# Optimization experiments

Hardware: AMD Instinct MI355X
Metric: run time of the kernel (lower is better)

Reference implementation:

```python
import jax, jax.numpy as jnp
import numpy as np

N = 100000
E = 1600000
NFEAT = 256
NHID = 128


def setup_inputs() -> dict:
    key = jax.random.key(0)
    k1, k2, k3, k4 = jax.random.split(key, 4)
    x = jax.random.normal(k1, (N, NFEAT), dtype=jnp.float32)
    edge_index = jax.random.randint(k2, (2, E), 0, N, dtype=jnp.int64)
    # GCNConv linear weight (stored as [nfeat, nhid] so h = x @ W) + bias
    W = jax.random.normal(k3, (NFEAT, NHID), dtype=jnp.float32) / np.sqrt(NFEAT)
    b = jnp.zeros((NHID,), dtype=jnp.float32)
    # PReLU single shared slope parameter (torch default init 0.25)
    prelu_a = jnp.asarray(0.25, dtype=jnp.float32)
    return {"x": x, "edge_index": edge_index, "W": W, "b": b, "prelu_a": prelu_a}


def _gcn_prelu(x, edge_index, W, b, prelu_a):
    n = x.shape[0]
    # spectral_norm reparametrization: divide weight by its largest singular value
    sigma = jnp.linalg.norm(W.astype(jnp.float32), ord=2)
    h = x @ (W / sigma)  # [N, nhid]
    # add self-loops (PyG GCNConv default)
    loop = jnp.arange(n, dtype=edge_index.dtype)
    row = jnp.concatenate([edge_index[0], loop])  # source
    col = jnp.concatenate([edge_index[1], loop])  # destination
    # symmetric degree normalization: deg from destination counts
    deg = jax.ops.segment_sum(jnp.ones_like(col, dtype=h.dtype), col, num_segments=n)
    dinv = jnp.where(deg > 0, jax.lax.rsqrt(deg), 0.0)
    norm = dinv[row] * dinv[col]  # [E+N]
    msgs = h[row] * norm[:, None]  # [E+N, nhid] gather
    out = jax.ops.segment_sum(msgs, col, num_segments=n) + b  # scatter-add
    # PReLU with shared slope
    return jnp.where(out > 0, out, prelu_a * out)


def reference(x, edge_index, W, b, prelu_a):
    return _gcn_prelu(x, edge_index, W, b, prelu_a)
```

## Files before the change

kernel.cpp:

```cpp
#include <hip/hip_runtime.h>

#define NN 100000
#define EE 1600000
#define NF 256
#define NH 128

#define BK 98
#define BNODE 1024
#define CHUNK 4096
#define NCHUNK ((EE + CHUNK - 1) / CHUNK)
#define CAP 24576

typedef unsigned int u32;
typedef unsigned short u16;
typedef __attribute__((ext_vector_type(8))) short short8;
typedef __attribute__((ext_vector_type(4))) float f32x4;

static __device__ __forceinline__ u16 f2bf(float f) {
  u32 u = __float_as_uint(f);
  u32 r = (u + 0x7FFFu + ((u >> 16) & 1u)) >> 16;
  return (u16)r;
}
static __device__ __forceinline__ float bflo(u32 u) { return __uint_as_float(u << 16); }
static __device__ __forceinline__ float bfhi(u32 u) { return __uint_as_float(u & 0xFFFF0000u); }

__global__ __launch_bounds__(256) void k_p0(const int* __restrict__ col,
                                            u32* __restrict__ hist2d) {
  __shared__ u32 hist[BK];
  int t = threadIdx.x;
  if (t < BK) hist[t] = 0;
  __syncthreads();
  int e0 = blockIdx.x * CHUNK;
  int e1 = min(e0 + CHUNK, EE);
  for (int e = e0 + t; e < e1; e += 256) {
    u32 d = (u32)col[e];
    atomicAdd(&hist[d >> 10], 1u);
  }
  __syncthreads();
  if (t < BK) hist2d[blockIdx.x * BK + t] = hist[t];
}

__global__ __launch_bounds__(256) void k_bs_spec(const u32* __restrict__ hist2d,
                                                 u32* __restrict__ bcnt,
                                                 u32* __restrict__ bbase,
                                                 u32* __restrict__ gcur,
                                                 u32* __restrict__ off,
                                                 const float* __restrict__ W,
                                                 u16* __restrict__ WtG,
                                                 float* __restrict__ sig) {
  __shared__ __align__(16) char MB[65536];
  __shared__ float diag[128];
  __shared__ float red[256];
  __shared__ float uvec[128];
  __shared__ float itrS;
  __shared__ int jmS;
  int t = threadIdx.x;

  if (blockIdx.x == 0) {
    u32* c = (u32*)MB;
    if (t < BK) {
      u32 s = 0;
      for (int ch = 0; ch < NCHUNK; ch++) s += hist2d[ch * BK + t];
      c[t] = s;
    }
    __syncthreads();
    if (t == 0) {
      u32 s = 0;
      for (int b2 = 0; b2 < BK; b2++) {
        bcnt[b2] = c[b2];
        bbase[b2] = s;
        gcur[b2] = s;
        s += c[b2];
      }
      off[NN] = EE;
    }
    return;
  }

  int l = t & 63, w = t >> 6;
  int p = l & 15, q = l >> 4;

  for (int base = t * 4; base < NF * NH; base += 256 * 4) {
    float4 v = *(const float4*)&W[base];
    int k = base >> 7, c0 = base & 127;
#pragma unroll
    for (int i = 0; i < 4; i++) {
      int c = c0 + i;
      int inner = (k * 2) ^ ((c & 7) << 4);
      *(u16*)(MB + c * 512 + inner) = f2bf(((const float*)&v)[i]);
    }
  }
  __syncthreads();
  for (int g = t; g < 128 * 128; g += 256) {
    int c = g >> 7, k = (g & 127) * 2;
    u32 val = *(u32*)(MB + c * 512 + ((k * 2) ^ ((c & 7) << 4)));
    ((u32*)WtG)[g] = val;
  }

  f32x4 acc[2][8] = {};
#pragma unroll
  for (int ks = 0; ks < 8; ks++) {
    int kb = (ks * 32 + q * 8) * 2;
    short8 afr[2], bfr[8];
#pragma unroll
    for (int m = 0; m < 2; m++) {
      int ra = w * 32 + m * 16 + p;
      afr[m] = *(const short8*)(MB + ra * 512 + (kb ^ ((ra & 7) << 4)));
    }
#pragma unroll
    for (int n = 0; n < 8; n++) {
      int r = n * 16 + p;
      bfr[n] = *(const short8*)(MB + r * 512 + (kb ^ ((r & 7) << 4)));
    }
#pragma unroll
    for (int m = 0; m < 2; m++)
#pragma unroll
      for (int n = 0; n < 8; n++)
        acc[m][n] = __builtin_amdgcn_mfma_f32_16x16x32_bf16(afr[m], bfr[n], acc[m][n], 0, 0, 0);
  }
#pragma unroll
  for (int m = 0; m < 2; m++)
#pragma unroll
    for (int n = 0; n < 8; n++)
#pragma unroll
      for (int g = 0; g < 4; g++) {
        int r = w * 32 + m * 16 + q * 4 + g;
        int c = n * 16 + p;
        if (r == c) diag[r] = acc[m][n][g];
      }
  __syncthreads();
  if (t == 0) {
    float s = 0.f;
    for (int i = 0; i < 128; i++) s += diag[i];
    itrS = 1.0f / s;
  }
  __syncthreads();
  {
    float itr = itrS;
    char* mb0 = MB;
#pragma unroll
    for (int m = 0; m < 2; m++)
#pragma unroll
      for (int n = 0; n < 8; n++)
#pragma unroll
        for (int g = 0; g < 4; g++) {
          int r = w * 32 + m * 16 + q * 4 + g;
          int c = n * 16 + p;
          *(u16*)(mb0 + r * 256 + ((c * 2) ^ ((r & 7) << 4))) = f2bf(acc[m][n][g] * itr);
        }
  }

  char* src = MB;
  char* dst = MB + 32768;
  for (int s = 0; s < 8; s++) {
    __syncthreads();
    f32x4 mac[2][8] = {};
#pragma unroll
    for (int ks = 0; ks < 4; ks++) {
      int kb = (ks * 32 + q * 8) * 2;
      short8 afr[2], bfr[8];
#pragma unroll
      for (int m = 0; m < 2; m++) {
        int ra = w * 32 + m * 16 + p;
        afr[m] = *(const short8*)(src + ra * 256 + (kb ^ ((ra & 7) << 4)));
      }
#pragma unroll
      for (int n = 0; n < 8; n++) {
        int r = n * 16 + p;
        bfr[n] = *(const short8*)(src + r * 256 + (kb ^ ((r & 7) << 4)));
      }
#pragma unroll
      for (int m = 0; m < 2; m++)
#pragma unroll
        for (int n = 0; n < 8; n++)
          mac[m][n] = __builtin_amdgcn_mfma_f32_16x16x32_bf16(afr[m], bfr[n], mac[m][n], 0, 0, 0);
    }
#pragma unroll
    for (int m = 0; m < 2; m++)
#pragma unroll
      for (int n = 0; n < 8; n++)
#pragma unroll
        for (int g = 0; g < 4; g++) {
          int r = w * 32 + m * 16 + q * 4 + g;
          int c = n * 16 + p;
          if (r == c) diag[r] = mac[m][n][g];
        }
    __syncthreads();
    if (t == 0) {
      float ss = 0.f;
      for (int i = 0; i < 128; i++) ss += diag[i];
      itrS = 1.0f / ss;
    }
    __syncthreads();
    float it2 = itrS;
#pragma unroll
    for (int m = 0; m < 2; m++)
#pragma unroll
      for (int n = 0; n < 8; n++)
#pragma unroll
        for (int g = 0; g < 4; g++) {
          int r = w * 32 + m * 16 + q * 4 + g;
          int c = n * 16 + p;
          *(u16*)(dst + r * 256 + ((c * 2) ^ ((r & 7) << 4))) = f2bf(mac[m][n][g] * it2);
        }
    char* tmp = src; src = dst; dst = tmp;
  }
  __syncthreads();

  if (t == 0) {
    int jm = 0;
    float bm = diag[0];
    for (int i = 1; i < 128; i++)
      if (diag[i] > bm) { bm = diag[i]; jm = i; }
    jmS = jm;
  }
  __syncthreads();
  int jm = jmS;
  if (t < 128) {
    u16 hv = *(u16*)(src + jm * 256 + ((t * 2) ^ ((jm & 7) << 4)));
    uvec[t] = __uint_as_float(((u32)hv) << 16);
  }
  __syncthreads();
  {
    float a2 = 0.f;
    const float* wr = &W[t * NH];
    for (int k = 0; k < NH; k++) a2 += wr[k] * uvec[k];
    red[t] = a2 * a2;
  }
  __syncthreads();
  if (t == 0) {
    float num = 0.f;
    for (int i = 0; i < 256; i++) num += red[i];
    float den = 0.f;
    for (int i = 0; i < 128; i++) den += uvec[i] * uvec[i];
    sig[0] = rsqrtf(num / den);
  }
}

__global__ __launch_bounds__(256) void k_p1(const int* __restrict__ row,
                                            const int* __restrict__ col,
                                            u32* __restrict__ gcur,
                                            u32* __restrict__ binned) {
  __shared__ u32 keybuf[CHUNK];
  __shared__ unsigned char bktbuf[CHUNK];
  __shared__ u32 hist[BK], lstart[BK], lofs[BK], gb[BK];
  int t = threadIdx.x;
  if (t < BK) hist[t] = 0;
  __syncthreads();
  int e0 = blockIdx.x * CHUNK;
  int n = min(CHUNK, EE - e0);
  for (int i = t; i < n; i += 256) {
    u32 d = (u32)col[e0 + i];
    atomicAdd(&hist[d >> 10], 1u);
  }
  __syncthreads();
  if (t == 0) {
    u32 s = 0;
    for (int b = 0; b < BK; b++) { lstart[b] = s; lofs[b] = s; s += hist[b]; }
  }
  __syncthreads();
  if (t < BK && hist[t]) gb[t] = atomicAdd(&gcur[t], hist[t]);
  __syncthreads();
  for (int i = t; i < n; i += 256) {
    u32 d = (u32)col[e0 + i];
    u32 s = (u32)row[e0 + i];
    u32 b = d >> 10;
    u32 p = atomicAdd(&lofs[b], 1u);
    keybuf[p] = ((d & 1023u) << 17) | s;
    bktbuf[p] = (unsigned char)b;
  }
  __syncthreads();
  for (int i = t; i < n; i += 256) {
    u32 b = bktbuf[i];
    binned[gb[b] + ((u32)i - lstart[b])] = keybuf[i];
  }
}

__global__ __launch_bounds__(1024) void k_p2(const u32* __restrict__ binned,
                                             const u32* __restrict__ bbase,
                                             const u32* __restrict__ bcnt,
                                             u32* __restrict__ off,
                                             float* __restrict__ dinv,
                                             int* __restrict__ csr) {
  __shared__ u32 hist[BNODE];
  __shared__ u32 loff[BNODE];
  __shared__ u32 cur[BNODE];
  __shared__ u32 stage[CAP];
  int b = blockIdx.x, t = threadIdx.x;
  u32 base = bbase[b], cnt = bcnt[b];
  hist[t] = 0;
  __syncthreads();
  for (u32 i = t; i < cnt; i += BNODE) {
    u32 key = binned[base + i];
    atomicAdd(&hist[key >> 17], 1u);
  }
  __syncthreads();
  u32 v = hist[t];
  loff[t] = v;
  __syncthreads();
  for (int d = 1; d < BNODE; d <<= 1) {
    u32 x = loff[t];
    u32 y = (t >= d) ? loff[t - d] : 0u;
    __syncthreads();
    loff[t] = x + y;
    __syncthreads();
  }
  u32 ex = loff[t] - v;
  cur[t] = ex;
  int g = b * BNODE + t;
  if (g < NN) {
    off[g] = base + ex;
    dinv[g] = rsqrtf((float)(v + 1u));
  }
  __syncthreads();
  if (cnt <= CAP) {
    for (u32 i = t; i < cnt; i += BNODE) {
      u32 key = binned[base + i];
      u32 p = atomicAdd(&cur[key >> 17], 1u);
      stage[p] = key & 0x1FFFFu;
    }
    __syncthreads();
    for (u32 i = t; i < cnt; i += BNODE) csr[base + i] = (int)stage[i];
  } else {
    for (u32 i = t; i < cnt; i += BNODE) {
      u32 key = binned[base + i];
      u32 p = atomicAdd(&cur[key >> 17], 1u);
      csr[base + p] = (int)(key & 0x1FFFFu);
    }
  }
}

__global__ __launch_bounds__(256) void k_mfma(const float* __restrict__ x,
                                              const u16* __restrict__ Wt,
                                              const float* __restrict__ dinv,
                                              u16* __restrict__ hs) {
  __shared__ __align__(16) u16 tile[128 * 128];
  int t = threadIdx.x;
  int l = t & 63, w = t >> 6;
  int row0 = blockIdx.x * 128;
  int lr = l & 15;
  int lk = (l >> 4) * 8;

  long arow[2];
#pragma unroll
  for (int m = 0; m < 2; m++) {
    int r = row0 + w * 32 + m * 16 + lr;
    arow[m] = (long)((r < NN) ? r : (NN - 1)) * NF;
  }

  f32x4 acc[2][8] = {};
  short8 afr[2][2];

#define LOADA(ph, k0)                                                        \
  {                                                                          \
    _Pragma("unroll") for (int m = 0; m < 2; m++) {                          \
      float4 p0 = *(const float4*)&x[arow[m] + (k0) + lk];                   \
      float4 p1 = *(const float4*)&x[arow[m] + (k0) + lk + 4];               \
      u32 wd[4];                                                             \
      wd[0] = (u32)f2bf(p0.x) | ((u32)f2bf(p0.y) << 16);                     \
      wd[1] = (u32)f2bf(p0.z) | ((u32)f2bf(p0.w) << 16);                     \
      wd[2] = (u32)f2bf(p1.x) | ((u32)f2bf(p1.y) << 16);                     \
      wd[3] = (u32)f2bf(p1.z) | ((u32)f2bf(p1.w) << 16);                     \
      afr[ph][m] = *(short8*)wd;                                             \
    }                                                                        \
  }

  LOADA(0, 0)
#pragma unroll
  for (int ks = 0; ks < 8; ks++) {
    int cur = ks & 1, nxt = cur ^ 1;
    if (ks < 7) LOADA(nxt, (ks + 1) * 32)
    short8 bfr[8];
#pragma unroll
    for (int n = 0; n < 8; n++)
      bfr[n] = *(const short8*)&Wt[(n * 16 + lr) * NF + ks * 32 + lk];
#pragma unroll
    for (int m = 0; m < 2; m++)
#pragma unroll
      for (int n = 0; n < 8; n++)
        acc[m][n] = __builtin_amdgcn_mfma_f32_16x16x32_bf16(afr[cur][m], bfr[n], acc[m][n], 0, 0, 0);
  }
#undef LOADA

#pragma unroll
  for (int m = 0; m < 2; m++) {
    int rbl = w * 32 + m * 16 + (l >> 4) * 4;
    float dv[4];
#pragma unroll
    for (int g = 0; g < 4; g++) {
      int r = row0 + rbl + g;
      dv[g] = (r < NN) ? dinv[r] : 0.f;
    }
#pragma unroll
    for (int n = 0; n < 8; n++)
#pragma unroll
      for (int g = 0; g < 4; g++)
        tile[(rbl + g) * 128 + n * 16 + lr] = f2bf(acc[m][n][g] * dv[g]);
  }
  __syncthreads();
  const uint4* tl = (const uint4*)tile;
  size_t outb = (size_t)row0 * NH;
#pragma unroll
  for (int k = 0; k < 8; k++) {
    int u = t + k * 256;
    if (row0 + (u >> 4) < NN) *(uint4*)&hs[outb + (size_t)u * 8] = tl[u];
  }
}

__global__ __launch_bounds__(256) void k_gather(const u16* __restrict__ hs,
                                                const int* __restrict__ csr,
                                                const u32* __restrict__ off,
                                                const float* __restrict__ dinv,
                                                const float* __restrict__ b,
                                                const float* __restrict__ pa,
                                                const float* __restrict__ sig,
                                                float* __restrict__ out) {
  int wid = threadIdx.x >> 6;
  int lane = threadIdx.x & 63;
  int n = blockIdx.x * 4 + wid;
  if (n >= NN) return;
  u32 s0 = off[n], s1 = off[n + 1];
  const u32* hrow = (const u32*)hs;
  float ax, ay;
  {
    u32 u = hrow[(size_t)n * 64 + lane];
    ax = bflo(u); ay = bfhi(u);
  }
  u32 e = s0;
  for (; e + 8 <= s1; e += 8) {
    int i0 = csr[e],     i1 = csr[e + 1], i2 = csr[e + 2], i3 = csr[e + 3];
    int i4 = csr[e + 4], i5 = csr[e + 5], i6 = csr[e + 6], i7 = csr[e + 7];
    u32 u0 = hrow[(size_t)i0 * 64 + lane];
    u32 u1 = hrow[(size_t)i1 * 64 + lane];
    u32 u2 = hrow[(size_t)i2 * 64 + lane];
    u32 u3 = hrow[(size_t)i3 * 64 + lane];
    u32 u4 = hrow[(size_t)i4 * 64 + lane];
    u32 u5 = hrow[(size_t)i5 * 64 + lane];
    u32 u6 = hrow[(size_t)i6 * 64 + lane];
    u32 u7 = hrow[(size_t)i7 * 64 + lane];
    ax += bflo(u0) + bflo(u1) + bflo(u2) + bflo(u3)
        + bflo(u4) + bflo(u5) + bflo(u6) + bflo(u7);
    ay += bfhi(u0) + bfhi(u1) + bfhi(u2) + bfhi(u3)
        + bfhi(u4) + bfhi(u5) + bfhi(u6) + bfhi(u7);
  }
  for (; e + 4 <= s1; e += 4) {
    int i0 = csr[e], i1 = csr[e + 1], i2 = csr[e + 2], i3 = csr[e + 3];
    u32 u0 = hrow[(size_t)i0 * 64 + lane];
    u32 u1 = hrow[(size_t)i1 * 64 + lane];
    u32 u2 = hrow[(size_t)i2 * 64 + lane];
    u32 u3 = hrow[(size_t)i3 * 64 + lane];
    ax += bflo(u0) + bflo(u1) + bflo(u2) + bflo(u3);
    ay += bfhi(u0) + bfhi(u1) + bfhi(u2) + bfhi(u3);
  }
  for (; e < s1; e++) {
    u32 u = hrow[(size_t)csr[e] * 64 + lane];
    ax += bflo(u); ay += bfhi(u);
  }
  float dv = dinv[n] * sig[0];
  float2 bb = *(const float2*)&b[lane * 2];
  float a = pa[0];
  float v0 = ax * dv + bb.x;
  float v1 = ay * dv + bb.y;
  float2 o;
  o.x = v0 > 0.f ? v0 : a * v0;
  o.y = v1 > 0.f ? v1 : a * v1;
  *(float2*)&out[(size_t)n * NH + lane * 2] = o;
}

extern "C" void kernel_launch(void* const* d_in, const int* in_sizes, int n_in,
                              void* d_out, int out_size, void* d_ws, size_t ws_size,
                              hipStream_t stream) {
  const float* x = (const float*)d_in[0];
  const int* ei = (const int*)d_in[1];
  const float* W = (const float*)d_in[2];
  const float* b = (const float*)d_in[3];
  const float* pa = (const float*)d_in[4];
  float* out = (float*)d_out;
  const int* row = ei;
  const int* col = ei + EE;

  char* base = (char*)d_ws;
  size_t o = 0;
  auto alloc = [&](size_t bytes) -> void* {
    void* p = base + o;
    o += (bytes + 63) & ~(size_t)63;
    return p;
  };
  u32* hist2d = (u32*)alloc((size_t)NCHUNK * BK * 4);
  u32* bcnt = (u32*)alloc(BK * 4);
  u32* bbase = (u32*)alloc(BK * 4);
  u32* gcur = (u32*)alloc(BK * 4);
  float* sig = (float*)alloc(64);
  float* dinv = (float*)alloc((size_t)NN * 4);
  u32* off = (u32*)alloc((size_t)(NN + 4) * 4);
  u32* binned = (u32*)alloc((size_t)EE * 4);
  int* csr = (int*)alloc((size_t)EE * 4);
  u16* Wt = (u16*)alloc((size_t)NF * NH * 2);
  u16* hs = (u16*)alloc((size_t)NN * NH * 2);
  (void)ws_size; (void)in_sizes; (void)n_in; (void)out_size;

  k_p0<<<NCHUNK, 256, 0, stream>>>(col, hist2d);
  k_bs_spec<<<2, 256, 0, stream>>>(hist2d, bcnt, bbase, gcur, off, W, Wt, sig);
  k_p1<<<NCHUNK, 256, 0, stream>>>(row, col, gcur, binned);
  k_p2<<<BK, BNODE, 0, stream>>>(binned, bbase, bcnt, off, dinv, csr);
  k_mfma<<<(NN + 127) / 128, 256, 0, stream>>>(x, Wt, dinv, hs);
  k_gather<<<(NN + 3) / 4, 256, 0, stream>>>(hs, csr, off, dinv, b, pa, sig, out);
}
```

Baseline: 202.5 us.

## Stage x tile in swizzled LDS and pre-permute W into MFMA fragment order

The GEMM kernel now loads the whole 128x256 x tile with coalesced float4 reads, converts it to bf16 and stores it into a swizzled 64KB LDS buffer. The MFMA loop then reads A fragments from LDS instead of doing strided per-lane global loads with register double-buffering. The weight matrix is written by the spectral-norm kernel in MFMA-fragment order, so each lane's B fragment load is contiguous. This trades the overlap of global loads with MFMA for better coalescing, and the 64KB LDS per block may lower occupancy.

After: 185.3 us. -8.5%, faster.

```diff
diff --git a/kernel.cpp b/kernel.cpp
--- a/kernel.cpp
+++ b/kernel.cpp
@@ -46,7 +46,7 @@
                                                  u32* __restrict__ gcur,
                                                  u32* __restrict__ off,
                                                  const float* __restrict__ W,
-                                                 u16* __restrict__ WtG,
+                                                 u16* __restrict__ Wt2,
                                                  float* __restrict__ sig) {
   __shared__ __align__(16) char MB[65536];
   __shared__ float diag[128];
@@ -91,10 +91,17 @@
     }
   }
   __syncthreads();
-  for (int g = t; g < 128 * 128; g += 256) {
-    int c = g >> 7, k = (g & 127) * 2;
-    u32 val = *(u32*)(MB + c * 512 + ((k * 2) ^ ((c & 7) << 4)));
-    ((u32*)WtG)[g] = val;
+  for (int u = t; u < 16384; u += 256) {
+    int h = u * 2;
+    int n = h >> 12;
+    int rem = h & 4095;
+    int ks = rem >> 9;
+    int rem2 = rem & 511;
+    int ll = rem2 >> 3;
+    int j = rem2 & 7;
+    int c = n * 16 + (ll & 15);
+    int k = ks * 32 + ((ll >> 4) << 3) + j;
+    ((u32*)Wt2)[u] = *(u32*)(MB + c * 512 + ((2 * k) ^ ((c & 7) << 4)));
   }
 
   f32x4 acc[2][8] = {};
@@ -331,57 +338,56 @@
 }
 
 __global__ __launch_bounds__(256) void k_mfma(const float* __restrict__ x,
-                                              const u16* __restrict__ Wt,
+                                              const u16* __restrict__ Wt2,
                                               const float* __restrict__ dinv,
                                               u16* __restrict__ hs) {
-  __shared__ __align__(16) u16 tile[128 * 128];
+  __shared__ __align__(16) char LB[65536];
   int t = threadIdx.x;
   int l = t & 63, w = t >> 6;
   int row0 = blockIdx.x * 128;
   int lr = l & 15;
   int lk = (l >> 4) * 8;
 
-  long arow[2];
-#pragma unroll
-  for (int m = 0; m < 2; m++) {
-    int r = row0 + w * 32 + m * 16 + lr;
-    arow[m] = (long)((r < NN) ? r : (NN - 1)) * NF;
-  }
-
+  const float4* x4 = (const float4*)x;
+#pragma unroll 4
+  for (int i = t; i < 128 * 64; i += 256) {
+    int r = i >> 6;
+    int cq = i & 63;
+    int gr = row0 + r;
+    if (gr >= NN) gr = NN - 1;
+    float4 v = x4[(size_t)gr * 64 + cq];
+    uint2 wv;
+    wv.x = (u32)f2bf(v.x) | ((u32)f2bf(v.y) << 16);
+    wv.y = (u32)f2bf(v.z) | ((u32)f2bf(v.w) << 16);
+    int kb = cq * 8;
+    *(uint2*)(LB + r * 512 + (kb ^ ((r & 7) << 4))) = wv;
+  }
+  __syncthreads();
+
+  int rbase = w * 32;
   f32x4 acc[2][8] = {};
-  short8 afr[2][2];
-
-#define LOADA(ph, k0)                                                        \
-  {                                                                          \
-    _Pragma("unroll") for (int m = 0; m < 2; m++) {                          \
-      float4 p0 = *(const float4*)&x[arow[m] + (k0) + lk];                   \
-      float4 p1 = *(const float4*)&x[arow[m] + (k0) + lk + 4];               \
-      u32 wd[4];                                                             \
-      wd[0] = (u32)f2bf(p0.x) | ((u32)f2bf(p0.y) << 16);                     \
-      wd[1] = (u32)f2bf(p0.z) | ((u32)f2bf(p0.w) << 16);                     \
-      wd[2] = (u32)f2bf(p1.x) | ((u32)f2bf(p1.y) << 16);                     \
-      wd[3] = (u32)f2bf(p1.z) | ((u32)f2bf(p1.w) << 16);                     \
-      afr[ph][m] = *(short8*)wd;                                             \
-    }                                                                        \
-  }
-
-  LOADA(0, 0)
 #pragma unroll
   for (int ks = 0; ks < 8; ks++) {
-    int cur = ks & 1, nxt = cur ^ 1;
-    if (ks < 7) LOADA(nxt, (ks + 1) * 32)
     short8 bfr[8];
 #pragma unroll
     for (int n = 0; n < 8; n++)
-      bfr[n] = *(const short8*)&Wt[(n * 16 + lr) * NF + ks * 32 + lk];
+      bfr[n] = *(const short8*)&Wt2[(size_t)(((n * 8 + ks) * 64) + l) * 8];
+    short8 afr[2];
+#pragma unroll
+    for (int m = 0; m < 2; m++) {
+      int r = rbase + m * 16 + lr;
+      int kb = (ks * 32 + lk) * 2;
+      afr[m] = *(const short8*)(LB + r * 512 + (kb ^ ((r & 7) << 4)));
+    }
 #pragma unroll
     for (int m = 0; m < 2; m++)
 #pragma unroll
       for (int n = 0; n < 8; n++)
-        acc[m][n] = __builtin_amdgcn_mfma_f32_16x16x32_bf16(afr[cur][m], bfr[n], acc[m][n], 0, 0, 0);
-  }
-#undef LOADA
-
+        acc[m][n] = __builtin_amdgcn_mfma_f32_16x16x32_bf16(afr[m], bfr[n], acc[m][n], 0, 0, 0);
+  }
+
+  __syncthreads();
+  u16* tile = (u16*)LB;
 #pragma unroll
   for (int m = 0; m < 2; m++) {
     int rbl = w * 32 + m * 16 + (l >> 4) * 4;
@@ -495,14 +501,14 @@
   u32* off = (u32*)alloc((size_t)(NN + 4) * 4);
   u32* binned = (u32*)alloc((size_t)EE * 4);
   int* csr = (int*)alloc((size_t)EE * 4);
-  u16* Wt = (u16*)alloc((size_t)NF * NH * 2);
+  u16* Wt2 = (u16*)alloc((size_t)NF * NH * 2);
   u16* hs = (u16*)alloc((size_t)NN * NH * 2);
   (void)ws_size; (void)in_sizes; (void)n_in; (void)out_size;
 
   k_p0<<<NCHUNK, 256, 0, stream>>>(col, hist2d);
-  k_bs_spec<<<2, 256, 0, stream>>>(hist2d, bcnt, bbase, gcur, off, W, Wt, sig);
+  k_bs_spec<<<2, 256, 0, stream>>>(hist2d, bcnt, bbase, gcur, off, W, Wt2, sig);
   k_p1<<<NCHUNK, 256, 0, stream>>>(row, col, gcur, binned);
   k_p2<<<BK, BNODE, 0, stream>>>(binned, bbase, bcnt, off, dinv, csr);
-  k_mfma<<<(NN + 127) / 128, 256, 0, stream>>>(x, Wt, dinv, hs);
+  k_mfma<<<(NN + 127) / 128, 256, 0, stream>>>(x, Wt2, dinv, hs);
   k_gather<<<(NN + 3) / 4, 256, 0, stream>>>(hs, csr, off, dinv, b, pa, sig, out);
 }
```
